# Optimization experiments

Measured on AMD Instinct MI355X. Metric: run time of the kernel, lower is better.

## Reference

```python
import jax, jax.numpy as jnp
import numpy as np

N = 200000
E = 6400000
NEG_SLOPE = 0.01  # nn.LeakyReLU default

def _leaky(x):
    return jnp.where(x >= 0, x, NEG_SLOPE * x)

def gcn_conv(x, edge_index, W, b, n):
    # PyG GCNConv: add self-loops, symmetric degree norm, linear, scatter-add, bias
    src, dst = edge_index[0], edge_index[1]
    loops = jnp.arange(n, dtype=src.dtype)
    src = jnp.concatenate([src, loops])
    dst = jnp.concatenate([dst, loops])
    deg = jax.ops.segment_sum(jnp.ones_like(dst, dtype=x.dtype), dst, num_segments=n)
    dinv = jnp.where(deg > 0, jax.lax.rsqrt(deg), 0.0)
    norm = dinv[src] * dinv[dst]                  # [E+N]
    h = x @ W.T                                   # [N,50] linear (no bias yet)
    msg = h[src] * norm[:, None]                  # gather + scale
    out = jax.ops.segment_sum(msg, dst, num_segments=n)  # scatter-add to targets
    return out + b

def setup_inputs() -> dict:
    key = jax.random.key(0)
    ks = jax.random.split(key, 20)
    def w(k, o, i):
        return jax.random.normal(k, (o, i), dtype=jnp.float32) * (1.0 / np.sqrt(i))
    def bvec(k, o):
        return jax.random.normal(k, (o,), dtype=jnp.float32) * 0.01
    inp = {
        'x': jax.random.normal(ks[0], (N, 150), dtype=jnp.float32),
        'edge_index': jax.random.randint(ks[1], (2, E), 0, N, dtype=jnp.int64 if jax.config.jax_enable_x64 else jnp.int32),
        'epsilon': jax.random.normal(ks[2], (N, 10), dtype=jnp.float32),
        'Wg': w(ks[3], 50, 50), 'bg': bvec(ks[4], 50),
        'We1': w(ks[5], 40, 50), 'be1': bvec(ks[6], 40),
        'We2': w(ks[7], 30, 40), 'be2': bvec(ks[8], 30),
        'We3': w(ks[9], 20, 30), 'be3': bvec(ks[10], 20),
        'Wfc': w(ks[11], 10, 10), 'bfc': bvec(ks[12], 10),
        'Wd1': w(ks[13], 20, 10), 'bd1': bvec(ks[14], 20),
        'Wd2': w(ks[15], 40, 20), 'bd2': bvec(ks[16], 40),
        'Wd3': w(ks[17], 50, 40), 'bd3': bvec(ks[18], 50),
    }
    return inp

def reference(x, edge_index, epsilon, Wg, bg, We1, be1, We2, be2, We3, be3,
              Wfc, bfc, Wd1, bd1, Wd2, bd2, Wd3, bd3):
    x1 = x[:, 100:]                                   # [N,50]
    h = gcn_conv(x1, edge_index, Wg, bg, x.shape[0])  # [N,50]
    # encoder
    e = _leaky(h @ We1.T + be1)
    e = _leaky(e @ We2.T + be2)
    e = e @ We3.T + be3                               # [N,20]
    mu, log_var = e[:, :10], e[:, 10:]
    # reparameterization: mu + eps * sqrt(exp(log_var))
    z1 = mu + epsilon * jnp.exp(0.5 * log_var)
    z = jax.nn.relu(z1 @ Wfc.T + bfc)                 # FC
    # decoder
    d = _leaky(z @ Wd1.T + bd1)
    d = _leaky(d @ Wd2.T + bd2)
    mu_prime = jax.nn.sigmoid(d @ Wd3.T + bd3)        # [N,50]
    return (mu_prime, mu, log_var, z)
```

## Files before the change

kernel.cpp:

```cpp
#include <hip/hip_runtime.h>


#define NEG 0.01f
#define GS 64
#define HS 56
#define ELLS 64
#define NB 16
#define SPILL_CAP 65536

#define DET_ES (1024 * 1024)
#define IS64_THRESH (DET_ES / 2)

#define META_INTS 1024

typedef int vint2 __attribute__((ext_vector_type(2)));
typedef _Float16 half4v __attribute__((ext_vector_type(4)));
typedef _Float16 half8v __attribute__((ext_vector_type(8)));

static __device__ __forceinline__ float bf2f(unsigned short u) {
    return __uint_as_float(((unsigned)u) << 16);
}
static __device__ __forceinline__ float leaky(float a) { return (a >= 0.f) ? a : NEG * a; }

__global__ void k_zero(int* __restrict__ indeg, int* __restrict__ flag,
                       int* __restrict__ meta, int n) {
    int i = blockIdx.x * 256 + threadIdx.x;
    if (i < n) indeg[i] = 0;
    if (blockIdx.x == 0) {
        for (int j = threadIdx.x; j < META_INTS; j += 256) meta[j] = 0;
        if (threadIdx.x == 0) { flag[0] = 0; flag[1] = 0; flag[2] = 0; }
    }
}

__global__ void k_detect(const unsigned* __restrict__ x, long xwords,
                         const unsigned* __restrict__ ei, long epairs,
                         int* __restrict__ flag) {
    int gw = (blockIdx.x * 256 + threadIdx.x) >> 6;
    int lane = threadIdx.x & 63;
    int side = gw >> 10;
    int ch = gw & 1023;
    int c = 0;
    if (side == 0) {
        long step = xwords >> 10;
        long base = (long)ch * step;
        if (base + 1024 > xwords) base = xwords > 1024 ? xwords - 1024 : 0;
#pragma unroll
        for (int t = 0; t < 16; t++) {
            long idx = base + t * 64 + lane;
            if (idx < xwords) {
                unsigned w = x[idx];
                if (((w >> 23) & 0xFFu) == 0xFFu || ((w >> 7) & 0xFFu) == 0xFFu) c++;
            }
        }
        for (int k = 32; k; k >>= 1) c += __shfl_xor(c, k);
        if (lane == 0 && c) atomicAdd(&flag[0], c);
    } else {
        long step = epairs >> 10;
        long base = (long)ch * step;
        if (base + 1024 > epairs) base = epairs > 1024 ? epairs - 1024 : 0;
#pragma unroll
        for (int t = 0; t < 16; t++) {
            long idx = base + t * 64 + lane;
            if (idx < epairs && ei[2 * idx + 1] == 0u) c++;
        }
        for (int k = 32; k; k >>= 1) c += __shfl_xor(c, k);
        if (lane == 0 && c) atomicAdd(&flag[1], c);
    }
}

__global__ __launch_bounds__(256) void k_hist(const int* __restrict__ ei,
                                              const int* __restrict__ flag,
                                              int* __restrict__ meta, int E, int N) {
    __shared__ int lh[NB];
    if (threadIdx.x < NB) lh[threadIdx.x] = 0;
    __syncthreads();
    bool is64 = flag[1] > IS64_THRESH;
    unsigned usw = ((unsigned)N + NB - 1) / NB;
    const long stride = 1024L * 256;
    if (is64) {
        const int2* p = (const int2*)ei;
        for (long e = (long)blockIdx.x * 256 + threadIdx.x; e < E; e += stride) {
            int d = p[E + e].x;
            if ((unsigned)d < (unsigned)N) atomicAdd(&lh[(unsigned)d / usw], 1);
        }
    } else {
        for (long e = (long)blockIdx.x * 256 + threadIdx.x; e < E; e += stride) {
            int d = ei[E + e];
            if ((unsigned)d < (unsigned)N) atomicAdd(&lh[(unsigned)d / usw], 1);
        }
    }
    __syncthreads();
    if (threadIdx.x < NB && lh[threadIdx.x]) atomicAdd(&meta[threadIdx.x * 16], lh[threadIdx.x]);
}

__global__ void k_scan(int* __restrict__ meta) {
    if (threadIdx.x == 0) {
        int acc = 0;
        for (int k = 0; k < NB; k++) {
            int c = meta[k * 16];
            meta[256 + k] = acc;
            meta[512 + k * 16] = acc;
            acc += c;
            meta[288 + k] = acc;
        }
    }
}

__global__ __launch_bounds__(256) void k_part(const int* __restrict__ ei,
                                              const int* __restrict__ flag,
                                              int* __restrict__ meta,
                                              int2* __restrict__ bucket, int E, int N) {
    __shared__ int2 buf[NB][512];
    __shared__ int lcnt[NB];
    __shared__ int lbase;
    if (threadIdx.x < NB) lcnt[threadIdx.x] = 0;
    __syncthreads();
    bool is64 = flag[1] > IS64_THRESH;
    unsigned usw = ((unsigned)N + NB - 1) / NB;
    int nsteps = (E + 2048 * 256 - 1) / (2048 * 256);
    for (int step = 0; step < nsteps; step++) {
        long e = (long)(step * 2048 + blockIdx.x) * 256 + threadIdx.x;
        int b = -1;
        int2 sd;
        if (e < E) {
            int src, d;
            if (is64) {
                const int2* p = (const int2*)ei;
                src = p[e].x;
                d = p[E + e].x;
            } else {
                src = ei[e];
                d = ei[E + e];
            }
            if ((unsigned)d < (unsigned)N) {
                b = (int)((unsigned)d / usw);
                sd = make_int2(src, d);
            }
        }
        if (b >= 0) {
            int p = atomicAdd(&lcnt[b], 1);
            buf[b][p] = sd;
        }
        __syncthreads();
        for (int k = 0; k < NB; k++) {
            int cnt = lcnt[k];
            if (cnt >= 256) {
                if (threadIdx.x == 0) lbase = atomicAdd(&meta[512 + k * 16], 256);
                __syncthreads();
                bucket[lbase + threadIdx.x] = buf[k][threadIdx.x];
                int rem = cnt - 256;
                int2 r;
                if (threadIdx.x < rem) r = buf[k][256 + threadIdx.x];
                __syncthreads();
                if (threadIdx.x < rem) buf[k][threadIdx.x] = r;
                if (threadIdx.x == 0) lcnt[k] = rem;
                __syncthreads();
            }
        }
    }
    for (int k = 0; k < NB; k++) {
        int cnt = lcnt[k];
        if (cnt > 0) {
            if (threadIdx.x == 0) lbase = atomicAdd(&meta[512 + k * 16], cnt);
            __syncthreads();
            if (threadIdx.x < cnt) bucket[lbase + threadIdx.x] = buf[k][threadIdx.x];
            __syncthreads();
        }
    }
}

__global__ __launch_bounds__(256) void k_build2(const int2* __restrict__ bucket,
                                                const int* __restrict__ meta,
                                                int* __restrict__ indeg,
                                                int* __restrict__ ebuf,
                                                int2* __restrict__ spill,
                                                int* __restrict__ flag, int N, int pass) {
    int s = pass * 8 + (blockIdx.x & 7);
    int q = blockIdx.x >> 3;
    int lo = meta[256 + s];
    int hi = meta[288 + s];
    for (int idx = lo + q * 256 + threadIdx.x; idx < hi; idx += 512 * 256) {
        vint2 t = __builtin_nontemporal_load((const vint2*)&bucket[idx]);
        int src = t.x;
        int d = t.y;
        if ((unsigned)src >= (unsigned)N) continue;
        int c = atomicAdd(&indeg[d], 1);
        if (c < ELLS) {
            ebuf[(size_t)d * ELLS + c] = src;
        } else {
            int o = atomicAdd(&flag[2], 1);
            if (o < SPILL_CAP) spill[o] = make_int2(src, d);
        }
    }
}

__global__ void k_dinv(const int* __restrict__ indeg, float* __restrict__ dinv, int n) {
    int i = blockIdx.x * 256 + threadIdx.x;
    if (i < n) dinv[i] = rsqrtf(1.0f + (float)indeg[i]);
}

struct CW {
    const void* src[16];
    int off[16];
    int n[16];
};
__global__ void k_convw(CW cw, float* __restrict__ dst, const int* __restrict__ flag) {
    int b = blockIdx.x;
    bool isf = flag[0] > 64;
    const float* sf = (const float*)cw.src[b];
    const unsigned short* sh = (const unsigned short*)cw.src[b];
    float* d = dst + cw.off[b];
    int n = cw.n[b];
    for (int i = threadIdx.x; i < n; i += 256) d[i] = isf ? sf[i] : bf2f(sh[i]);
}

#define O_WG 0
#define O_BG 2500
#define O_WE1 2550
#define O_BE1 4550
#define O_WE2 4590
#define O_BE2 5790
#define O_WE3 5820
#define O_BE3 6420
#define O_WFC 6440
#define O_BFC 6540
#define O_WD1 6550
#define O_BD1 6750
#define O_WD2 6770
#define O_BD2 7570
#define O_WD3 7610
#define O_BD3 9610
#define W_TOT 9660

__global__ __launch_bounds__(256) void k_g(const void* __restrict__ xv,
                                           const float* __restrict__ W,
                                           const float* __restrict__ dinv,
                                           const int* __restrict__ flag,
                                           _Float16* __restrict__ g16, int n) {
    int i = blockIdx.x * 256 + threadIdx.x;
    if (i >= n) return;
    bool isf = flag[0] > 64;
    float xr[50];
    if (isf) {
        const float2* p = (const float2*)((const float*)xv + (size_t)i * 150 + 100);
#pragma unroll
        for (int k = 0; k < 25; k++) {
            float2 q = p[k];
            xr[2 * k] = q.x;
            xr[2 * k + 1] = q.y;
        }
    } else {
        const unsigned* p = (const unsigned*)((const unsigned short*)xv + (size_t)i * 150 + 100);
#pragma unroll
        for (int k = 0; k < 25; k++) {
            unsigned u = p[k];
            xr[2 * k] = __uint_as_float(u << 16);
            xr[2 * k + 1] = __uint_as_float(u & 0xFFFF0000u);
        }
    }
    const float* Wg = W + O_WG;
    float di = dinv[i];
    float o[64];
#pragma unroll
    for (int f = 0; f < 50; f += 2) {
        float a0 = 0.f, a1 = 0.f;
#pragma unroll
        for (int p = 0; p < 50; p++) {
            a0 += Wg[f * 50 + p] * xr[p];
            a1 += Wg[(f + 1) * 50 + p] * xr[p];
        }
        o[f] = a0 * di;
        o[f + 1] = a1 * di;
    }
#pragma unroll
    for (int f = 50; f < 64; f++) o[f] = 0.f;
    half8v* gr8 = (half8v*)(g16 + (size_t)i * GS);
#pragma unroll
    for (int p = 0; p < 8; p++) {
        half8v hv;
#pragma unroll
        for (int q = 0; q < 8; q++) hv[q] = (_Float16)o[8 * p + q];
        gr8[p] = hv;
    }
}

__global__ __launch_bounds__(256) void k_gather(const _Float16* __restrict__ g16,
                                                const int* __restrict__ indeg,
                                                const int* __restrict__ ebuf,
                                                const float* __restrict__ dinv,
                                                const float* __restrict__ W,
                                                float* __restrict__ h1, int n) {
    int wid = threadIdx.x >> 6;
    int lane = threadIdx.x & 63;
    int i = blockIdx.x * 4 + wid;
    if (i >= n) return;
    int q = lane >> 4;
    int r = lane & 15;
    int cnt = indeg[i];
    if (cnt > ELLS) cnt = ELLS;
    int ev = (lane < cnt) ? ebuf[(size_t)i * ELLS + lane] : 0;
    const half4v* g4 = (const half4v*)g16;
    float4 a0 = make_float4(0.f, 0.f, 0.f, 0.f);
    float4 a1 = a0, a2 = a0, a3 = a0;
    int m = 0;
    for (; m + 16 <= cnt; m += 16) {
        int j0 = __shfl(ev, m + q);
        int j1 = __shfl(ev, m + 4 + q);
        int j2 = __shfl(ev, m + 8 + q);
        int j3 = __shfl(ev, m + 12 + q);
        half4v t0 = g4[(size_t)j0 * 16 + r];
        half4v t1 = g4[(size_t)j1 * 16 + r];
        half4v t2 = g4[(size_t)j2 * 16 + r];
        half4v t3 = g4[(size_t)j3 * 16 + r];
        a0.x += (float)t0.x; a0.y += (float)t0.y; a0.z += (float)t0.z; a0.w += (float)t0.w;
        a1.x += (float)t1.x; a1.y += (float)t1.y; a1.z += (float)t1.z; a1.w += (float)t1.w;
        a2.x += (float)t2.x; a2.y += (float)t2.y; a2.z += (float)t2.z; a2.w += (float)t2.w;
        a3.x += (float)t3.x; a3.y += (float)t3.y; a3.z += (float)t3.z; a3.w += (float)t3.w;
    }
    for (; m + 4 <= cnt; m += 4) {
        int j = __shfl(ev, m + q);
        half4v t = g4[(size_t)j * 16 + r];
        a0.x += (float)t.x; a0.y += (float)t.y; a0.z += (float)t.z; a0.w += (float)t.w;
    }
    if (m < cnt) {
        int j = __shfl(ev, m + q);
        if (m + q < cnt) {
            half4v t = g4[(size_t)j * 16 + r];
            a0.x += (float)t.x; a0.y += (float)t.y; a0.z += (float)t.z; a0.w += (float)t.w;
        }
    }
    float4 s;
    s.x = (a0.x + a1.x) + (a2.x + a3.x);
    s.y = (a0.y + a1.y) + (a2.y + a3.y);
    s.z = (a0.z + a1.z) + (a2.z + a3.z);
    s.w = (a0.w + a1.w) + (a2.w + a3.w);
    s.x += __shfl_xor(s.x, 16); s.y += __shfl_xor(s.y, 16);
    s.z += __shfl_xor(s.z, 16); s.w += __shfl_xor(s.w, 16);
    s.x += __shfl_xor(s.x, 32); s.y += __shfl_xor(s.y, 32);
    s.z += __shfl_xor(s.z, 32); s.w += __shfl_xor(s.w, 32);
    if (lane < 16) {
        float di = dinv[i];
        half4v self = g4[(size_t)i * 16 + lane];
        float4 b = ((const float4*)(W + O_BG))[lane];
        float4 h;
        h.x = (s.x + (float)self.x) * di + b.x;
        h.y = (s.y + (float)self.y) * di + b.y;
        h.z = (s.z + (float)self.z) * di + b.z;
        h.w = (s.w + (float)self.w) * di + b.w;
        float* hr = h1 + (size_t)i * HS;
        if (lane < 12) {
            ((float4*)hr)[lane] = h;
        } else if (lane == 12) {
            hr[48] = h.x;
            hr[49] = h.y;
        }
    }
}

__global__ void k_spill(const int2* __restrict__ spill, const int* __restrict__ flag,
                        const _Float16* __restrict__ g16, const float* __restrict__ dinv,
                        float* __restrict__ h1) {
    int nov = flag[2];
    if (nov > SPILL_CAP) nov = SPILL_CAP;
    int lane = threadIdx.x & 63;
    int wave = (blockIdx.x * 256 + threadIdx.x) >> 6;
    for (int e = wave; e < nov; e += gridDim.x * 4) {
        int2 sd = spill[e];
        if (lane < 50)
            atomicAdd(&h1[(size_t)sd.y * HS + lane],
                      (float)g16[(size_t)sd.x * GS + lane] * dinv[sd.y]);
    }
}


__global__ __launch_bounds__(256) void k_e1(const float* __restrict__ h1,
                                            const float* __restrict__ W,
                                            float* __restrict__ t1, int n) {
    int i = blockIdx.x * 256 + threadIdx.x;
    if (i >= n) return;
    float v0[50];
    const float* hr = h1 + (size_t)i * HS;
    const float4* hr4 = (const float4*)hr;
#pragma unroll
    for (int p = 0; p < 12; p++) {
        float4 t = hr4[p];
        v0[4 * p] = t.x; v0[4 * p + 1] = t.y; v0[4 * p + 2] = t.z; v0[4 * p + 3] = t.w;
    }
    v0[48] = hr[48];
    v0[49] = hr[49];
    float o[40];
#pragma unroll
    for (int f = 0; f < 40; f++) {
        float a = W[O_BE1 + f];
#pragma unroll
        for (int p = 0; p < 50; p++) a += W[O_WE1 + f * 50 + p] * v0[p];
        o[f] = leaky(a);
    }
    float4* ot = (float4*)(t1 + (size_t)i * 40);
#pragma unroll
    for (int p = 0; p < 10; p++) ot[p] = make_float4(o[4 * p], o[4 * p + 1], o[4 * p + 2], o[4 * p + 3]);
}

__global__ __launch_bounds__(256) void k_e23(const float* __restrict__ t1,
                                             const float* __restrict__ W,
                                             float* __restrict__ out, int n) {
    int i = blockIdx.x * 256 + threadIdx.x;
    if (i >= n) return;
    float v1[40];
    const float4* tr = (const float4*)(t1 + (size_t)i * 40);
#pragma unroll
    for (int p = 0; p < 10; p++) {
        float4 q = tr[p];
        v1[4 * p] = q.x; v1[4 * p + 1] = q.y; v1[4 * p + 2] = q.z; v1[4 * p + 3] = q.w;
    }
    float v2[30];
#pragma unroll
    for (int f = 0; f < 30; f++) {
        float a = W[O_BE2 + f];
#pragma unroll
        for (int p = 0; p < 40; p++) a += W[O_WE2 + f * 40 + p] * v1[p];
        v2[f] = leaky(a);
    }
    float v3[20];
#pragma unroll
    for (int f = 0; f < 20; f++) {
        float a = W[O_BE3 + f];
#pragma unroll
        for (int p = 0; p < 30; p++) a += W[O_WE3 + f * 30 + p] * v2[p];
        v3[f] = a;
    }
    float2* o_mu = (float2*)(out + (size_t)n * 50 + (size_t)i * 10);
    float2* o_lv = (float2*)(out + (size_t)n * 60 + (size_t)i * 10);
#pragma unroll
    for (int p = 0; p < 5; p++) {
        o_mu[p] = make_float2(v3[2 * p], v3[2 * p + 1]);
        o_lv[p] = make_float2(v3[10 + 2 * p], v3[10 + 2 * p + 1]);
    }
}

__global__ __launch_bounds__(256) void k_zfc(float* outb,
                                             const void* __restrict__ epsv,
                                             const float* __restrict__ W,
                                             const int* __restrict__ flag,
                                             float* __restrict__ t3, int n) {
    int i = blockIdx.x * 256 + threadIdx.x;
    if (i >= n) return;
    bool isf = flag[0] > 64;
    float mu[10], lv[10];
    const float2* pm = (const float2*)(outb + (size_t)n * 50 + (size_t)i * 10);
    const float2* pl = (const float2*)(outb + (size_t)n * 60 + (size_t)i * 10);
#pragma unroll
    for (int p = 0; p < 5; p++) {
        float2 a = pm[p]; mu[2 * p] = a.x; mu[2 * p + 1] = a.y;
        float2 b = pl[p]; lv[2 * p] = b.x; lv[2 * p + 1] = b.y;
    }
    float ev[10];
    if (isf) {
        const float* p = (const float*)epsv + (size_t)i * 10;
#pragma unroll
        for (int k = 0; k < 10; k++) ev[k] = p[k];
    } else {
        const unsigned short* p = (const unsigned short*)epsv + (size_t)i * 10;
#pragma unroll
        for (int k = 0; k < 10; k++) ev[k] = bf2f(p[k]);
    }
    float z1[10];
#pragma unroll
    for (int k = 0; k < 10; k++) z1[k] = mu[k] + ev[k] * expf(0.5f * lv[k]);
    float z[10];
#pragma unroll
    for (int f = 0; f < 10; f++) {
        float a = W[O_BFC + f];
#pragma unroll
        for (int p = 0; p < 10; p++) a += W[O_WFC + f * 10 + p] * z1[p];
        z[f] = (a > 0.f) ? a : 0.f;
    }
    float2* o_z = (float2*)(outb + (size_t)n * 70 + (size_t)i * 10);
#pragma unroll
    for (int p = 0; p < 5; p++) o_z[p] = make_float2(z[2 * p], z[2 * p + 1]);
    float d1[20];
#pragma unroll
    for (int f = 0; f < 20; f++) {
        float a = W[O_BD1 + f];
#pragma unroll
        for (int p = 0; p < 10; p++) a += W[O_WD1 + f * 10 + p] * z[p];
        d1[f] = leaky(a);
    }
    float d2[40];
#pragma unroll
    for (int f = 0; f < 40; f++) {
        float a = W[O_BD2 + f];
#pragma unroll
        for (int p = 0; p < 20; p++) a += W[O_WD2 + f * 20 + p] * d1[p];
        d2[f] = leaky(a);
    }
    float4* ot = (float4*)(t3 + (size_t)i * 40);
#pragma unroll
    for (int p = 0; p < 10; p++)
        ot[p] = make_float4(d2[4 * p], d2[4 * p + 1], d2[4 * p + 2], d2[4 * p + 3]);
}

__global__ __launch_bounds__(256) void k_d3(const float* __restrict__ t3,
                                            const float* __restrict__ W,
                                            float* __restrict__ out, int n) {
    int i = blockIdx.x * 256 + threadIdx.x;
    if (i >= n) return;
    float d2[40];
    const float4* tr = (const float4*)(t3 + (size_t)i * 40);
#pragma unroll
    for (int p = 0; p < 10; p++) {
        float4 q = tr[p];
        d2[4 * p] = q.x; d2[4 * p + 1] = q.y; d2[4 * p + 2] = q.z; d2[4 * p + 3] = q.w;
    }
    float o[50];
#pragma unroll
    for (int f = 0; f < 50; f++) {
        float a = W[O_BD3 + f];
#pragma unroll
        for (int p = 0; p < 40; p++) a += W[O_WD3 + f * 40 + p] * d2[p];
        o[f] = 1.f / (1.f + expf(-a));
    }
    float2* om = (float2*)(out + (size_t)i * 50);
#pragma unroll
    for (int p = 0; p < 25; p++) om[p] = make_float2(o[2 * p], o[2 * p + 1]);
}

extern "C" void kernel_launch(void* const* d_in, const int* in_sizes, int n_in,
                              void* d_out, int out_size, void* d_ws, size_t ws_size,
                              hipStream_t stream) {
    const int N = in_sizes[0] / 150;
    const int E = in_sizes[1] / 2;

    char* w = (char*)d_ws;
    auto alloc = [&](size_t bytes) {
        void* p = (void*)w;
        w += (bytes + 255) & ~(size_t)255;
        return p;
    };
    int* indeg = (int*)alloc((size_t)N * 4);
    int* flag = (int*)alloc(256);
    int* meta = (int*)alloc((size_t)META_INTS * 4);
    float* dinv = (float*)alloc((size_t)N * 4);
    float* Wall = (float*)alloc((size_t)W_TOT * 4);
    int2* spill = (int2*)alloc((size_t)SPILL_CAP * 8);
    _Float16* g16 = (_Float16*)alloc((size_t)N * GS * 2);
    float* h1 = (float*)alloc((size_t)N * HS * 4);
    int* ebuf = (int*)alloc((size_t)N * ELLS * 4);

    int2* bucket;
    if ((size_t)E * 8 <= (size_t)N * GS * 2 + (size_t)N * HS * 4) {
        bucket = (int2*)g16;
    } else {
        bucket = (int2*)alloc((size_t)E * 8);
    }

    float* t1 = (float*)ebuf;
    float* t3 = h1;

    CW cw;
    static const int wn[16] = {2500, 50, 2000, 40, 1200, 30, 600, 20,
                               100, 10, 200, 20, 800, 40, 2000, 50};
    static const int wo[16] = {O_WG, O_BG, O_WE1, O_BE1, O_WE2, O_BE2, O_WE3, O_BE3,
                               O_WFC, O_BFC, O_WD1, O_BD1, O_WD2, O_BD2, O_WD3, O_BD3};
    for (int k = 0; k < 16; k++) {
        cw.src[k] = d_in[3 + k];
        cw.off[k] = wo[k];
        cw.n[k] = wn[k];
    }

    int nbN = (N + 255) / 256;

    k_zero<<<nbN, 256, 0, stream>>>(indeg, flag, meta, N);
    k_detect<<<512, 256, 0, stream>>>((const unsigned*)d_in[0], (long)N * 75,
                                      (const unsigned*)d_in[1], (long)E, flag);
    k_hist<<<1024, 256, 0, stream>>>((const int*)d_in[1], flag, meta, E, N);
    k_scan<<<1, 64, 0, stream>>>(meta);
    k_part<<<2048, 256, 0, stream>>>((const int*)d_in[1], flag, meta, bucket, E, N);
    k_build2<<<4096, 256, 0, stream>>>(bucket, meta, indeg, ebuf, spill, flag, N, 0);
    k_build2<<<4096, 256, 0, stream>>>(bucket, meta, indeg, ebuf, spill, flag, N, 1);
    k_dinv<<<nbN, 256, 0, stream>>>(indeg, dinv, N);
    k_convw<<<16, 256, 0, stream>>>(cw, Wall, flag);
    k_g<<<nbN, 256, 0, stream>>>(d_in[0], Wall, dinv, flag, g16, N);
    k_gather<<<(N + 3) / 4, 256, 0, stream>>>(g16, indeg, ebuf, dinv, Wall, h1, N);
    k_spill<<<64, 256, 0, stream>>>(spill, flag, g16, dinv, h1);
    k_e1<<<nbN, 256, 0, stream>>>(h1, Wall, t1, N);
    k_e23<<<nbN, 256, 0, stream>>>(t1, Wall, (float*)d_out, N);
    k_zfc<<<nbN, 256, 0, stream>>>((float*)d_out, d_in[2], Wall, flag, t3, N);
    k_d3<<<nbN, 256, 0, stream>>>(t3, Wall, (float*)d_out, N);
}
```

Measured before the change: 980.6 us.

## Pack bucketed edges into 32-bit words, double bucket count, prefetch next edge

```diff
diff --git a/kernel.cpp b/kernel.cpp
--- a/kernel.cpp
+++ b/kernel.cpp
@@ -5,22 +5,22 @@
 #define GS 64
 #define HS 56
 #define ELLS 64
-#define NB 16
+#define NB 32
 #define SPILL_CAP 65536
+#define SENT 0x7FFFFFFF
 
 #define DET_ES (1024 * 1024)
 #define IS64_THRESH (DET_ES / 2)
 
 #define META_INTS 1024
 
-typedef int vint2 __attribute__((ext_vector_type(2)));
+static __device__ __forceinline__ float bf2f(unsigned short u) {
+    return __uint_as_float(((unsigned)u) << 16);
+}
+static __device__ __forceinline__ float leaky(float a) { return (a >= 0.f) ? a : NEG * a; }
+
 typedef _Float16 half4v __attribute__((ext_vector_type(4)));
 typedef _Float16 half8v __attribute__((ext_vector_type(8)));
-
-static __device__ __forceinline__ float bf2f(unsigned short u) {
-    return __uint_as_float(((unsigned)u) << 16);
-}
-static __device__ __forceinline__ float leaky(float a) { return (a >= 0.f) ? a : NEG * a; }
 
 __global__ void k_zero(int* __restrict__ indeg, int* __restrict__ flag,
                        int* __restrict__ meta, int n) {
@@ -98,10 +98,10 @@
         int acc = 0;
         for (int k = 0; k < NB; k++) {
             int c = meta[k * 16];
-            meta[256 + k] = acc;
-            meta[512 + k * 16] = acc;
+            meta[520 + k] = acc;
+            meta[640 + k * 8] = acc;
             acc += c;
-            meta[288 + k] = acc;
+            meta[560 + k] = acc;
         }
     }
 }
@@ -109,8 +109,8 @@
 __global__ __launch_bounds__(256) void k_part(const int* __restrict__ ei,
                                               const int* __restrict__ flag,
                                               int* __restrict__ meta,
-                                              int2* __restrict__ bucket, int E, int N) {
-    __shared__ int2 buf[NB][512];
+                                              int* __restrict__ bucket, int E, int N) {
+    __shared__ int buf[NB][512];
     __shared__ int lcnt[NB];
     __shared__ int lbase;
     if (threadIdx.x < NB) lcnt[threadIdx.x] = 0;
@@ -118,38 +118,40 @@
     bool is64 = flag[1] > IS64_THRESH;
     unsigned usw = ((unsigned)N + NB - 1) / NB;
     int nsteps = (E + 2048 * 256 - 1) / (2048 * 256);
+    int psrc = 0, pd = -1;
+    {
+        long e = (long)blockIdx.x * 256 + threadIdx.x;
+        if (e < E) {
+            if (is64) { const int2* p = (const int2*)ei; psrc = p[e].x; pd = p[E + e].x; }
+            else      { psrc = ei[e]; pd = ei[E + e]; }
+        }
+    }
     for (int step = 0; step < nsteps; step++) {
-        long e = (long)(step * 2048 + blockIdx.x) * 256 + threadIdx.x;
-        int b = -1;
-        int2 sd;
-        if (e < E) {
-            int src, d;
-            if (is64) {
-                const int2* p = (const int2*)ei;
-                src = p[e].x;
-                d = p[E + e].x;
-            } else {
-                src = ei[e];
-                d = ei[E + e];
+        int csrc = psrc, cd = pd;
+        pd = -1;
+        if (step + 1 < nsteps) {
+            long e = (long)((step + 1) * 2048 + blockIdx.x) * 256 + threadIdx.x;
+            if (e < E) {
+                if (is64) { const int2* p = (const int2*)ei; psrc = p[e].x; pd = p[E + e].x; }
+                else      { psrc = ei[e]; pd = ei[E + e]; }
             }
-            if ((unsigned)d < (unsigned)N) {
-                b = (int)((unsigned)d / usw);
-                sd = make_int2(src, d);
-            }
-        }
-        if (b >= 0) {
+        }
+        if ((unsigned)cd < (unsigned)N) {
+            int b = (int)((unsigned)cd / usw);
+            int dl = cd - b * (int)usw;
+            int u = ((unsigned)csrc >= (unsigned)N) ? SENT : ((dl << 18) | csrc);
             int p = atomicAdd(&lcnt[b], 1);
-            buf[b][p] = sd;
+            buf[b][p] = u;
         }
         __syncthreads();
         for (int k = 0; k < NB; k++) {
             int cnt = lcnt[k];
             if (cnt >= 256) {
-                if (threadIdx.x == 0) lbase = atomicAdd(&meta[512 + k * 16], 256);
+                if (threadIdx.x == 0) lbase = atomicAdd(&meta[640 + k * 8], 256);
                 __syncthreads();
                 bucket[lbase + threadIdx.x] = buf[k][threadIdx.x];
                 int rem = cnt - 256;
-                int2 r;
+                int r;
                 if (threadIdx.x < rem) r = buf[k][256 + threadIdx.x];
                 __syncthreads();
                 if (threadIdx.x < rem) buf[k][threadIdx.x] = r;
@@ -161,7 +163,7 @@
     for (int k = 0; k < NB; k++) {
         int cnt = lcnt[k];
         if (cnt > 0) {
-            if (threadIdx.x == 0) lbase = atomicAdd(&meta[512 + k * 16], cnt);
+            if (threadIdx.x == 0) lbase = atomicAdd(&meta[640 + k * 8], cnt);
             __syncthreads();
             if (threadIdx.x < cnt) bucket[lbase + threadIdx.x] = buf[k][threadIdx.x];
             __syncthreads();
@@ -169,7 +171,7 @@
     }
 }
 
-__global__ __launch_bounds__(256) void k_build2(const int2* __restrict__ bucket,
+__global__ __launch_bounds__(256) void k_build2(const int* __restrict__ bucket,
                                                 const int* __restrict__ meta,
                                                 int* __restrict__ indeg,
                                                 int* __restrict__ ebuf,
@@ -177,13 +179,15 @@
                                                 int* __restrict__ flag, int N, int pass) {
     int s = pass * 8 + (blockIdx.x & 7);
     int q = blockIdx.x >> 3;
-    int lo = meta[256 + s];
-    int hi = meta[288 + s];
+    int sw = (N + NB - 1) / NB;
+    int nlo = s * sw;
+    int lo = meta[520 + s];
+    int hi = meta[560 + s];
     for (int idx = lo + q * 256 + threadIdx.x; idx < hi; idx += 512 * 256) {
-        vint2 t = __builtin_nontemporal_load((const vint2*)&bucket[idx]);
-        int src = t.x;
-        int d = t.y;
-        if ((unsigned)src >= (unsigned)N) continue;
+        int u = __builtin_nontemporal_load(&bucket[idx]);
+        if (u == SENT) continue;
+        int src = u & 0x3FFFF;
+        int d = nlo + (int)((unsigned)u >> 18);
         int c = atomicAdd(&indeg[d], 1);
         if (c < ELLS) {
             ebuf[(size_t)d * ELLS + c] = src;
@@ -547,11 +551,11 @@
     float* h1 = (float*)alloc((size_t)N * HS * 4);
     int* ebuf = (int*)alloc((size_t)N * ELLS * 4);
 
-    int2* bucket;
-    if ((size_t)E * 8 <= (size_t)N * GS * 2 + (size_t)N * HS * 4) {
-        bucket = (int2*)g16;
+    int* bucket;
+    if ((size_t)E * 4 <= (size_t)N * GS * 2 + (size_t)N * HS * 4) {
+        bucket = (int*)g16;
     } else {
-        bucket = (int2*)alloc((size_t)E * 8);
+        bucket = (int*)alloc((size_t)E * 4);
     }
 
     float* t1 = (float*)ebuf;
@@ -578,6 +582,8 @@
     k_part<<<2048, 256, 0, stream>>>((const int*)d_in[1], flag, meta, bucket, E, N);
     k_build2<<<4096, 256, 0, stream>>>(bucket, meta, indeg, ebuf, spill, flag, N, 0);
     k_build2<<<4096, 256, 0, stream>>>(bucket, meta, indeg, ebuf, spill, flag, N, 1);
+    k_build2<<<4096, 256, 0, stream>>>(bucket, meta, indeg, ebuf, spill, flag, N, 2);
+    k_build2<<<4096, 256, 0, stream>>>(bucket, meta, indeg, ebuf, spill, flag, N, 3);
     k_dinv<<<nbN, 256, 0, stream>>>(indeg, dinv, N);
     k_convw<<<16, 256, 0, stream>>>(cw, Wall, flag);
     k_g<<<nbN, 256, 0, stream>>>(d_in[0], Wall, dinv, flag, g16, N);
```

Result: slower. 1.068 ms (+8.9%).
